# Kernel optimization log

Hardware: AMD Instinct MI355X
Metric: run time of the kernel (lower is better)

The kernel has to match this reference:

```python
import jax, jax.numpy as jnp
import numpy as np

VOCAB, DIM = 100000, 300
B, L = 4096, 200
HIDDEN, OUT = 1000, 3


def setup_inputs() -> dict:
    key = jax.random.key(0)
    k_emb, k_x, k_len, k_w1, k_b1, k_w2, k_b2 = jax.random.split(key, 7)
    emb_table = jax.random.normal(k_emb, (VOCAB, DIM), dtype=jnp.float32)
    x = jax.random.randint(k_x, (B, L), 0, VOCAB)
    lengths = jax.random.randint(k_len, (B,), 1, L + 1)  # >=1 to avoid div-by-zero
    W1 = jax.random.normal(k_w1, (2 * DIM, HIDDEN), dtype=jnp.float32) * 0.02
    b1 = jax.random.normal(k_b1, (HIDDEN,), dtype=jnp.float32) * 0.02
    W2 = jax.random.normal(k_w2, (HIDDEN, OUT), dtype=jnp.float32) * 0.02
    b2 = jax.random.normal(k_b2, (OUT,), dtype=jnp.float32) * 0.02
    return {"emb_table": emb_table, "W1": W1, "b1": b1, "W2": W2, "b2": b2,
            "x": x, "lengths": lengths}


def reference(emb_table, W1, b1, W2, b2, x, lengths):
    emb = emb_table[x]                                   # [B, L, D] gather
    # Faithful to original: mean uses sum over ALL positions (incl. padding)
    mean_pooled = jnp.sum(emb, axis=1) / lengths[:, None].astype(emb.dtype)  # [B, D]
    # Max only over the first `length` real tokens
    mask = jnp.arange(L)[None, :] < lengths[:, None]     # [B, L]
    neg_inf = jnp.array(-jnp.inf, dtype=emb.dtype)
    max_pooled = jnp.max(jnp.where(mask[:, :, None], emb, neg_inf), axis=1)  # [B, D]
    rep = jnp.concatenate([mean_pooled, max_pooled], axis=1)  # [B, 2D]
    h = jax.nn.relu(rep @ W1 + b1)                       # [B, 1000]
    return h @ W2 + b2                                   # [B, OUT]
```

## Files before the change

kernel.cpp:

```cpp
#include <hip/hip_runtime.h>
#include <math.h>

#define VOCAB  100000
#define DIM    300
#define IDIM   320
#define BB     4096
#define LL     200
#define HIDDEN 1000
#define OUTC   3
#define KT     19
#define NT     64
#define MTILES (BB / 16)

#define QSCALE (6.0f / 127.0f)
#define QINV   (127.0f / 6.0f)

#define W1_BLKS   ((KT * NT * 64 + 255) / 256)
#define INIT_BLKS ((BB * OUTC + 255) / 256)
#define CONV_BLKS ((VOCAB * 20 + 255) / 256)

typedef __attribute__((ext_vector_type(8))) short  short8;
typedef __attribute__((ext_vector_type(4))) float  floatx4;
typedef __attribute__((ext_vector_type(2))) unsigned short ushort2v;

__device__ inline ushort f2bf(float f) {
    union { float f; unsigned u; } v; v.f = f;
    unsigned u = v.u;
    u += 0x7fffu + ((u >> 16) & 1u);
    return (ushort)(u >> 16);
}
__device__ inline float4 f4max(float4 a, float4 b) {
    return make_float4(fmaxf(a.x, b.x), fmaxf(a.y, b.y), fmaxf(a.z, b.z), fmaxf(a.w, b.w));
}
__device__ inline float4 f4add(float4 a, float4 b) {
    return make_float4(a.x + b.x, a.y + b.y, a.z + b.z, a.w + b.w);
}
__device__ inline unsigned pkmax16(unsigned a, unsigned b) {
    union { unsigned u; ushort2v v; } x, y, r;
    x.u = a; y.u = b;
    r.v = __builtin_elementwise_max(x.v, y.v);
    return r.u;
}

__device__ inline int a_slot(int k, int ml) {
    const int kt = k >> 5, kk = k & 31;
    return ((kt << 6) + ml + ((kk >> 3) << 4)) * 8 + (kk & 7);
}

__device__ inline unsigned q4(float a, float b, float c, float d) {
    int q0 = min(max(__float2int_rn(a * QINV) + 128, 0), 255);
    int q1 = min(max(__float2int_rn(b * QINV) + 128, 0), 255);
    int q2 = min(max(__float2int_rn(c * QINV) + 128, 0), 255);
    int q3 = min(max(__float2int_rn(d * QINV) + 128, 0), 255);
    return (unsigned)q0 | ((unsigned)q1 << 8) | ((unsigned)q2 << 16) | ((unsigned)q3 << 24);
}

__device__ inline void acc_sm(const uint4& raw, unsigned* sLo, unsigned* sHi,
                              unsigned* mLo, unsigned* mHi) {
    const unsigned* ww = (const unsigned*)&raw;
    #pragma unroll
    for (int w = 0; w < 4; ++w) {
        const unsigned u  = ww[w];
        const unsigned lo = u & 0x00FF00FFu;
        const unsigned hi = (u >> 8) & 0x00FF00FFu;
        sLo[w] += lo;  sHi[w] += hi;
        mLo[w] = pkmax16(mLo[w], lo);
        mHi[w] = pkmax16(mHi[w], hi);
    }
}
__device__ inline void acc_s(const uint4& raw, unsigned* sLo, unsigned* sHi) {
    const unsigned* ww = (const unsigned*)&raw;
    #pragma unroll
    for (int w = 0; w < 4; ++w) {
        const unsigned u = ww[w];
        sLo[w] += u & 0x00FF00FFu;
        sHi[w] += (u >> 8) & 0x00FF00FFu;
    }
}

__global__ __launch_bounds__(256) void prep_all(
    const float* __restrict__ emb, unsigned char* __restrict__ embQ,
    const float* __restrict__ W1,  ushort* __restrict__ w1p,
    const float* __restrict__ b2,  float* __restrict__ out)
{
    const int bid = blockIdx.x;
    const int tid = threadIdx.x;
    if (bid < W1_BLKS) {
        const int g = bid * 256 + tid;
        if (g >= KT * NT * 64) return;
        const int lane = g & 63;
        const int nt   = (g >> 6) & (NT - 1);
        const int kt   = g >> 12;
        const int n    = nt * 16 + (lane & 15);
        const int kb   = kt * 32 + ((lane >> 4) << 3);
        short8 v;
        #pragma unroll
        for (int j = 0; j < 8; ++j) {
            const int k = kb + j;
            const float f = (k < 600 && n < HIDDEN) ? W1[k * HIDDEN + n] : 0.f;
            v[j] = (short)f2bf(f);
        }
        ((short8*)w1p)[g] = v;
    } else if (bid < W1_BLKS + INIT_BLKS) {
        const int g = (bid - W1_BLKS) * 256 + tid;
        if (g < BB * OUTC) out[g] = b2[g % OUTC];
    } else {
        const int g = (bid - W1_BLKS - INIT_BLKS) * 256 + tid;
        if (g >= VOCAB * 20) return;
        const int row = g / 20;
        const int c   = g - row * 20;
        const float4* rp = (const float4*)(emb + (size_t)row * DIM);
        uint4 o;
        unsigned* ow = (unsigned*)&o;
        #pragma unroll
        for (int v = 0; v < 4; ++v) {
            const int fi = 4 * c + v;
            float4 f = (fi < 75) ? rp[fi] : make_float4(0.f, 0.f, 0.f, 0.f);
            ow[v] = q4(f.x, f.y, f.z, f.w);
        }
        *(uint4*)(embQ + (size_t)g * 16) = o;
    }
}

__global__ __launch_bounds__(256, 8) void gather_pool_i8(
    const unsigned char* __restrict__ embQ,
    const int*           __restrict__ x,
    const int*           __restrict__ lengths,
    ushort*              __restrict__ repA)
{
    __shared__ int      xS[LL];
    __shared__ unsigned pS[3][20][8];
    __shared__ unsigned pM[3][20][8];

    const int tid  = threadIdx.x;
    const int lane = tid & 63;
    const int wave = tid >> 6;
    const int row  = blockIdx.x;

    for (int i = tid; i < LL; i += 256) xS[i] = x[row * LL + i];
    const int len = lengths[row];
    __syncthreads();

    const int  t0   = wave * 50;
    const int  vmax = min(max(len - t0, 0), 50);
    const bool ga   = (lane < 20);
    const bool ld   = (lane < 40);
    const int  lg   = ga ? lane : (lane - 20);
    const unsigned char* base = embQ + 16 * lg;

    unsigned sLo[4], sHi[4], mLo[4], mHi[4];
    #pragma unroll
    for (int w = 0; w < 4; ++w) { sLo[w] = sHi[w] = 0u; mLo[w] = mHi[w] = 0u; }

    const int full = vmax >> 1;
    int p = 0;
    for (; p + 2 <= full; p += 2) {
        const int tA = t0 + 2 * p;
        const int i0 = ga ? xS[tA]     : xS[tA + 1];
        const int i1 = ga ? xS[tA + 2] : xS[tA + 3];
        uint4 r0 = make_uint4(0,0,0,0), r1 = make_uint4(0,0,0,0);
        if (ld) {
            r0 = *(const uint4*)(base + (size_t)i0 * IDIM);
            r1 = *(const uint4*)(base + (size_t)i1 * IDIM);
        }
        acc_sm(r0, sLo, sHi, mLo, mHi);
        acc_sm(r1, sLo, sHi, mLo, mHi);
    }
    if (p < full) {
        const int tA = t0 + 2 * p;
        const int i0 = ga ? xS[tA] : xS[tA + 1];
        uint4 r0 = make_uint4(0,0,0,0);
        if (ld) r0 = *(const uint4*)(base + (size_t)i0 * IDIM);
        acc_sm(r0, sLo, sHi, mLo, mHi);
        ++p;
    }
    if (vmax & 1) {
        const int tA = t0 + 2 * p;
        const int i0 = ga ? xS[tA] : xS[tA + 1];
        uint4 r0 = make_uint4(0,0,0,0);
        if (ld) r0 = *(const uint4*)(base + (size_t)i0 * IDIM);
        const unsigned* ww = (const unsigned*)&r0;
        #pragma unroll
        for (int w = 0; w < 4; ++w) {
            const unsigned u  = ww[w];
            const unsigned lo = u & 0x00FF00FFu;
            const unsigned hi = (u >> 8) & 0x00FF00FFu;
            sLo[w] += lo;  sHi[w] += hi;
            if (ga) { mLo[w] = pkmax16(mLo[w], lo); mHi[w] = pkmax16(mHi[w], hi); }
        }
        ++p;
    }
    for (; p + 2 <= 25; p += 2) {
        const int tA = t0 + 2 * p;
        const int i0 = ga ? xS[tA]     : xS[tA + 1];
        const int i1 = ga ? xS[tA + 2] : xS[tA + 3];
        uint4 r0 = make_uint4(0,0,0,0), r1 = make_uint4(0,0,0,0);
        if (ld) {
            r0 = *(const uint4*)(base + (size_t)i0 * IDIM);
            r1 = *(const uint4*)(base + (size_t)i1 * IDIM);
        }
        acc_s(r0, sLo, sHi);
        acc_s(r1, sLo, sHi);
    }
    if (p < 25) {
        const int tA = t0 + 2 * p;
        const int i0 = ga ? xS[tA] : xS[tA + 1];
        uint4 r0 = make_uint4(0,0,0,0);
        if (ld) r0 = *(const uint4*)(base + (size_t)i0 * IDIM);
        acc_s(r0, sLo, sHi);
    }

    {
        const int src = ga ? (lane + 20) : lane;
        #pragma unroll
        for (int w = 0; w < 4; ++w) {
            sLo[w] += (unsigned)__shfl((int)sLo[w], src);
            sHi[w] += (unsigned)__shfl((int)sHi[w], src);
            mLo[w] = pkmax16(mLo[w], (unsigned)__shfl((int)mLo[w], src));
            mHi[w] = pkmax16(mHi[w], (unsigned)__shfl((int)mHi[w], src));
        }
    }

    if (wave != 0 && ga) {
        #pragma unroll
        for (int w = 0; w < 4; ++w) {
            pS[wave - 1][lane][w]     = sLo[w];
            pS[wave - 1][lane][4 + w] = sHi[w];
            pM[wave - 1][lane][w]     = mLo[w];
            pM[wave - 1][lane][4 + w] = mHi[w];
        }
    }
    __syncthreads();
    if (wave == 0 && ga) {
        #pragma unroll
        for (int wv = 0; wv < 3; ++wv)
            #pragma unroll
            for (int w = 0; w < 4; ++w) {
                sLo[w] += pS[wv][lane][w];
                sHi[w] += pS[wv][lane][4 + w];
                mLo[w] = pkmax16(mLo[w], pM[wv][lane][w]);
                mHi[w] = pkmax16(mHi[w], pM[wv][lane][4 + w]);
            }

        float s[16], m[16];
        #pragma unroll
        for (int w = 0; w < 4; ++w) {
            s[4*w+0] = (float)(sLo[w] & 0xFFFFu);
            s[4*w+2] = (float)(sLo[w] >> 16);
            s[4*w+1] = (float)(sHi[w] & 0xFFFFu);
            s[4*w+3] = (float)(sHi[w] >> 16);
            m[4*w+0] = (float)(mLo[w] & 0xFFFFu);
            m[4*w+2] = (float)(mLo[w] >> 16);
            m[4*w+1] = (float)(mHi[w] & 0xFFFFu);
            m[4*w+3] = (float)(mHi[w] >> 16);
        }

        const float c1 = QSCALE / (float)len;
        const int mt = row >> 4;
        const int ml = row & 15;
        ushort* rb = repA + (size_t)mt * (KT * 512);

        ushort mv[16];
        #pragma unroll
        for (int j = 0; j < 16; ++j) mv[j] = f2bf((m[j] - 128.f) * QSCALE);

        if (lane < 18) {
            #pragma unroll
            for (int h = 0; h < 2; ++h) {
                short8 q;
                #pragma unroll
                for (int j = 0; j < 8; ++j)
                    q[j] = (short)f2bf((s[8*h + j] - 25600.f) * c1);
                *(short8*)(rb + a_slot(16 * lane + 8 * h, ml)) = q;
            }
            #pragma unroll
            for (int h = 0; h < 2; ++h) {
                const int k0 = 300 + 16 * lane + 8 * h;
                *(ushort4*)(rb + a_slot(k0, ml)) =
                    make_ushort4(mv[8*h+0], mv[8*h+1], mv[8*h+2], mv[8*h+3]);
                *(ushort4*)(rb + a_slot(k0 + 4, ml)) =
                    make_ushort4(mv[8*h+4], mv[8*h+5], mv[8*h+6], mv[8*h+7]);
            }
        } else if (lane == 18) {
            short8 q;
            #pragma unroll
            for (int j = 0; j < 8; ++j) q[j] = (short)f2bf((s[j] - 25600.f) * c1);
            *(short8*)(rb + a_slot(288, ml)) = q;
            *(ushort4*)(rb + a_slot(296, ml)) =
                make_ushort4(f2bf((s[8] - 25600.f) * c1), f2bf((s[9] - 25600.f) * c1),
                             f2bf((s[10] - 25600.f) * c1), f2bf((s[11] - 25600.f) * c1));
            *(ushort4*)(rb + a_slot(588, ml)) = make_ushort4(mv[0], mv[1], mv[2], mv[3]);
            *(ushort4*)(rb + a_slot(592, ml)) = make_ushort4(mv[4], mv[5], mv[6], mv[7]);
            *(ushort4*)(rb + a_slot(596, ml)) = make_ushort4(mv[8], mv[9], mv[10], mv[11]);
            *(ushort4*)(rb + a_slot(600, ml)) = make_ushort4(0, 0, 0, 0);
        } else {
            *(ushort4*)(rb + a_slot(604, ml)) = make_ushort4(0, 0, 0, 0);
        }
    }
}

__global__ __launch_bounds__(256, 8) void gather_pool_f32(
    const float* __restrict__ emb,
    const int*   __restrict__ x,
    const int*   __restrict__ lengths,
    ushort*      __restrict__ repA)
{
    __shared__ int    xS[LL];
    __shared__ float4 pS[3][75];
    __shared__ float4 pM[3][75];

    const int tid  = threadIdx.x;
    const int lane = tid & 63;
    const int wave = tid >> 6;
    const int row  = blockIdx.x;

    for (int i = tid; i < LL; i += 256) xS[i] = x[row * LL + i];
    const int len = lengths[row];
    __syncthreads();

    const int  t0   = wave * (LL / 4);
    const int  vmax = min(max(len - t0, 0), LL / 4);
    const bool tl   = (lane < 11);
    const float4 z4 = make_float4(0.f, 0.f, 0.f, 0.f);

    float4 s4 = z4, st = z4;
    float4 m4 = make_float4(-INFINITY, -INFINITY, -INFINITY, -INFINITY);
    float4 mt = m4;

    int t = 0;
    #pragma unroll 4
    for (; t < vmax; ++t) {
        const int idx = xS[t0 + t];
        const float4* rp = (const float4*)(emb + (size_t)idx * DIM);
        float4 a = rp[lane];
        float4 b = tl ? rp[64 + lane] : z4;
        s4 = f4add(s4, a); st = f4add(st, b);
        m4 = f4max(m4, a); mt = f4max(mt, b);
    }
    #pragma unroll 4
    for (; t < LL / 4; ++t) {
        const int idx = xS[t0 + t];
        const float4* rp = (const float4*)(emb + (size_t)idx * DIM);
        float4 a = rp[lane];
        float4 b = tl ? rp[64 + lane] : z4;
        s4 = f4add(s4, a); st = f4add(st, b);
    }

    if (wave != 0) {
        pS[wave - 1][lane] = s4; pM[wave - 1][lane] = m4;
        if (tl) { pS[wave - 1][64 + lane] = st; pM[wave - 1][64 + lane] = mt; }
    }
    __syncthreads();
    if (wave == 0) {
        #pragma unroll
        for (int w = 0; w < 3; ++w) {
            s4 = f4add(s4, pS[w][lane]); m4 = f4max(m4, pM[w][lane]);
            if (tl) { st = f4add(st, pS[w][64 + lane]); mt = f4max(mt, pM[w][64 + lane]); }
        }
        const float inv = 1.0f / (float)len;
        const int mtile = row >> 4;
        const int ml    = row & 15;
        ushort* rb = repA + (size_t)mtile * (KT * 512);
        {
            ushort4 q = make_ushort4(f2bf(s4.x*inv), f2bf(s4.y*inv), f2bf(s4.z*inv), f2bf(s4.w*inv));
            *(ushort4*)(rb + a_slot(4 * lane, ml)) = q;
        }
        {
            ushort4 q = make_ushort4(f2bf(m4.x), f2bf(m4.y), f2bf(m4.z), f2bf(m4.w));
            *(ushort4*)(rb + a_slot(300 + 4 * lane, ml)) = q;
        }
        if (tl) {
            ushort4 q1 = make_ushort4(f2bf(st.x*inv), f2bf(st.y*inv), f2bf(st.z*inv), f2bf(st.w*inv));
            *(ushort4*)(rb + a_slot(256 + 4 * lane, ml)) = q1;
            ushort4 q2 = make_ushort4(f2bf(mt.x), f2bf(mt.y), f2bf(mt.z), f2bf(mt.w));
            *(ushort4*)(rb + a_slot(556 + 4 * lane, ml)) = q2;
        }
        if (lane >= 56) rb[a_slot(600 + (lane - 56), ml)] = 0;
    }
}

__global__ __launch_bounds__(256, 4) void mlp_mfma(
    const ushort* __restrict__ w1p,
    const ushort* __restrict__ repA,
    const float*  __restrict__ bias1,
    const float*  __restrict__ W2,
    float*        __restrict__ out)
{
    __shared__ short8 aS[2 * KT * 64];

    const int tid  = threadIdx.x;
    const int lane = tid & 63;
    const int wave = tid >> 6;
    const int mp   = blockIdx.x >> 3;
    const int e    = blockIdx.x & 7;

    {
        const short8* ap = (const short8*)(repA + (size_t)(2 * mp) * (KT * 512));
        for (int i = tid; i < 2 * KT * 64; i += 256) aS[i] = ap[i];
    }
    __syncthreads();

    const int nt0 = e * 8 + wave;
    const int nt1 = nt0 + 4;
    const short8* bp = (const short8*)w1p;

    floatx4 acc[2][2];
    #pragma unroll
    for (int mi = 0; mi < 2; ++mi)
        #pragma unroll
        for (int s = 0; s < 2; ++s) acc[mi][s] = (floatx4){0.f, 0.f, 0.f, 0.f};

    #pragma unroll
    for (int kt = 0; kt < KT; ++kt) {
        const short8 av0 = aS[kt * 64 + lane];
        const short8 av1 = aS[KT * 64 + kt * 64 + lane];
        const short8 bv0 = bp[(kt * NT + nt0) * 64 + lane];
        const short8 bv1 = bp[(kt * NT + nt1) * 64 + lane];
        acc[0][0] = __builtin_amdgcn_mfma_f32_16x16x32_bf16(av0, bv0, acc[0][0], 0, 0, 0);
        acc[0][1] = __builtin_amdgcn_mfma_f32_16x16x32_bf16(av0, bv1, acc[0][1], 0, 0, 0);
        acc[1][0] = __builtin_amdgcn_mfma_f32_16x16x32_bf16(av1, bv0, acc[1][0], 0, 0, 0);
        acc[1][1] = __builtin_amdgcn_mfma_f32_16x16x32_bf16(av1, bv1, acc[1][1], 0, 0, 0);
    }
    __syncthreads();
    float* red = (float*)aS;

    float po[2][4][3];
    #pragma unroll
    for (int mi = 0; mi < 2; ++mi)
        #pragma unroll
        for (int rg = 0; rg < 4; ++rg)
            #pragma unroll
            for (int j = 0; j < OUTC; ++j) po[mi][rg][j] = 0.f;

    #pragma unroll
    for (int s = 0; s < 2; ++s) {
        const int n = (s ? nt1 : nt0) * 16 + (lane & 15);
        const bool valid = (n < HIDDEN);
        const float bb  = bias1[valid ? n : 0];
        const float w20 = valid ? W2[n * 3 + 0] : 0.f;
        const float w21 = valid ? W2[n * 3 + 1] : 0.f;
        const float w22 = valid ? W2[n * 3 + 2] : 0.f;
        #pragma unroll
        for (int mi = 0; mi < 2; ++mi)
            #pragma unroll
            for (int rg = 0; rg < 4; ++rg) {
                const float h = fmaxf(acc[mi][s][rg] + bb, 0.f);
                po[mi][rg][0] = fmaf(h, w20, po[mi][rg][0]);
                po[mi][rg][1] = fmaf(h, w21, po[mi][rg][1]);
                po[mi][rg][2] = fmaf(h, w22, po[mi][rg][2]);
            }
    }

    #pragma unroll
    for (int mi = 0; mi < 2; ++mi)
        #pragma unroll
        for (int rg = 0; rg < 4; ++rg)
            #pragma unroll
            for (int j = 0; j < OUTC; ++j) {
                float v = po[mi][rg][j];
                v += __shfl_xor(v, 1);
                v += __shfl_xor(v, 2);
                v += __shfl_xor(v, 4);
                v += __shfl_xor(v, 8);
                if ((lane & 15) == 0)
                    red[(wave * 32 + mi * 16 + (lane >> 4) * 4 + rg) * 3 + j] = v;
            }
    __syncthreads();

    if (tid < 32 * OUTC) {
        const int m = tid / OUTC, j = tid % OUTC;
        const float s = red[(0 * 32 + m) * 3 + j] + red[(1 * 32 + m) * 3 + j]
                      + red[(2 * 32 + m) * 3 + j] + red[(3 * 32 + m) * 3 + j];
        atomicAdd(&out[(size_t)(mp * 32 + m) * OUTC + j], s);
    }
}

extern "C" void kernel_launch(void* const* d_in, const int* in_sizes, int n_in,
                              void* d_out, int out_size, void* d_ws, size_t ws_size,
                              hipStream_t stream) {
    const float* emb = (const float*)d_in[0];
    const float* W1  = (const float*)d_in[1];
    const float* b1  = (const float*)d_in[2];
    const float* W2  = (const float*)d_in[3];
    const float* b2  = (const float*)d_in[4];
    const int*   x   = (const int*)d_in[5];
    const int*   len = (const int*)d_in[6];
    float* out = (float*)d_out;

    const size_t W1P_ELTS  = (size_t)KT * NT * 64 * 8;
    const size_t REPA_ELTS = (size_t)MTILES * KT * 512;
    ushort* w1p  = (ushort*)d_ws;
    ushort* repA = w1p + W1P_ELTS;
    unsigned char* embQ = (unsigned char*)(repA + REPA_ELTS);
    const size_t need = (W1P_ELTS + REPA_ELTS) * 2 + (size_t)VOCAB * IDIM;
    const bool doConv = (ws_size >= need);

    const int prepGrid = W1_BLKS + INIT_BLKS + (doConv ? CONV_BLKS : 0);
    hipLaunchKernelGGL(prep_all, dim3(prepGrid), dim3(256), 0, stream,
                       emb, embQ, W1, w1p, b2, out);
    if (doConv) {
        hipLaunchKernelGGL(gather_pool_i8, dim3(BB), dim3(256), 0, stream,
                           embQ, x, len, repA);
    } else {
        hipLaunchKernelGGL(gather_pool_f32, dim3(BB), dim3(256), 0, stream,
                           emb, x, len, repA);
    }
    hipLaunchKernelGGL(mlp_mfma, dim3((MTILES / 2) * 8), dim3(256), 0, stream,
                       w1p, repA, b1, W2, out);
}
```

Baseline: 256.9 us.

## Fuse MLP into gather kernel via last-block-per-tile election

The int8 gather/pool kernel now counts finished rows per 16-row tile with an atomic counter. The last block to finish a tile then runs the full MLP for that tile with MFMA and atomically adds the results to the output, which removes the separate MLP launch and its pass over repA. The fallback MLP kernel is retiled to 16-row tiles split four ways across hidden columns. The cost is that only 256 elected blocks do the MLP, each computing all 1000 hidden units serially with 4 waves. Lowering the launch bound to 4 blocks per SM may also reduce gather occupancy.

```diff
diff --git a/kernel.cpp b/kernel.cpp
--- a/kernel.cpp
+++ b/kernel.cpp
@@ -81,7 +81,8 @@
 __global__ __launch_bounds__(256) void prep_all(
     const float* __restrict__ emb, unsigned char* __restrict__ embQ,
     const float* __restrict__ W1,  ushort* __restrict__ w1p,
-    const float* __restrict__ b2,  float* __restrict__ out)
+    const float* __restrict__ b2,  float* __restrict__ out,
+    int* __restrict__ cnt)
 {
     const int bid = blockIdx.x;
     const int tid = threadIdx.x;
@@ -104,6 +105,7 @@
     } else if (bid < W1_BLKS + INIT_BLKS) {
         const int g = (bid - W1_BLKS) * 256 + tid;
         if (g < BB * OUTC) out[g] = b2[g % OUTC];
+        if (g < MTILES) cnt[g] = 0;
     } else {
         const int g = (bid - W1_BLKS - INIT_BLKS) * 256 + tid;
         if (g >= VOCAB * 20) return;
@@ -122,15 +124,23 @@
     }
 }
 
-__global__ __launch_bounds__(256, 8) void gather_pool_i8(
+__global__ __launch_bounds__(256, 4) void gather_mlp_i8(
     const unsigned char* __restrict__ embQ,
     const int*           __restrict__ x,
     const int*           __restrict__ lengths,
-    ushort*              __restrict__ repA)
+    ushort*              __restrict__ repA,
+    const ushort*        __restrict__ w1p,
+    const float*         __restrict__ bias1,
+    const float*         __restrict__ W2,
+    float*               __restrict__ out,
+    int*                 __restrict__ cnt)
 {
-    __shared__ int      xS[LL];
-    __shared__ unsigned pS[3][20][8];
-    __shared__ unsigned pM[3][20][8];
+    __shared__ __attribute__((aligned(16))) char shbuf[KT * 64 * 16];
+    __shared__ int electFlag;
+
+    int*      xS  = (int*)shbuf;
+    unsigned* pSf = (unsigned*)(shbuf + 800);
+    unsigned* pMf = (unsigned*)(shbuf + 2720);
 
     const int tid  = threadIdx.x;
     const int lane = tid & 63;
@@ -224,10 +234,10 @@
     if (wave != 0 && ga) {
         #pragma unroll
         for (int w = 0; w < 4; ++w) {
-            pS[wave - 1][lane][w]     = sLo[w];
-            pS[wave - 1][lane][4 + w] = sHi[w];
-            pM[wave - 1][lane][w]     = mLo[w];
-            pM[wave - 1][lane][4 + w] = mHi[w];
+            pSf[((wave - 1) * 20 + lane) * 8 + w]     = sLo[w];
+            pSf[((wave - 1) * 20 + lane) * 8 + 4 + w] = sHi[w];
+            pMf[((wave - 1) * 20 + lane) * 8 + w]     = mLo[w];
+            pMf[((wave - 1) * 20 + lane) * 8 + 4 + w] = mHi[w];
         }
     }
     __syncthreads();
@@ -236,10 +246,10 @@
         for (int wv = 0; wv < 3; ++wv)
             #pragma unroll
             for (int w = 0; w < 4; ++w) {
-                sLo[w] += pS[wv][lane][w];
-                sHi[w] += pS[wv][lane][4 + w];
-                mLo[w] = pkmax16(mLo[w], pM[wv][lane][w]);
-                mHi[w] = pkmax16(mHi[w], pM[wv][lane][4 + w]);
+                sLo[w] += pSf[(wv * 20 + lane) * 8 + w];
+                sHi[w] += pSf[(wv * 20 + lane) * 8 + 4 + w];
+                mLo[w] = pkmax16(mLo[w], pMf[(wv * 20 + lane) * 8 + w]);
+                mHi[w] = pkmax16(mHi[w], pMf[(wv * 20 + lane) * 8 + 4 + w]);
             }
 
         float s[16], m[16];
@@ -297,6 +307,88 @@
             *(ushort4*)(rb + a_slot(604, ml)) = make_ushort4(0, 0, 0, 0);
         }
     }
+
+    if (tid == 0) {
+        __threadfence();
+        electFlag = (atomicAdd(&cnt[row >> 4], 1) == 15) ? 1 : 0;
+    }
+    __syncthreads();
+    if (!electFlag) return;
+    __threadfence();
+
+    const int g = row >> 4;
+    short8* aS = (short8*)shbuf;
+    {
+        const short8* ap = (const short8*)(repA + (size_t)g * (KT * 512));
+        for (int i = tid; i < KT * 64; i += 256) aS[i] = ap[i];
+    }
+    __syncthreads();
+
+    float po[4][3];
+    #pragma unroll
+    for (int rg = 0; rg < 4; ++rg)
+        #pragma unroll
+        for (int j = 0; j < OUTC; ++j) po[rg][j] = 0.f;
+
+    const short8* bp = (const short8*)w1p;
+    #pragma unroll
+    for (int c = 0; c < 4; ++c) {
+        const int nt0 = wave * 16 + c * 4;
+        floatx4 acc[4];
+        #pragma unroll
+        for (int s2 = 0; s2 < 4; ++s2) acc[s2] = (floatx4){0.f, 0.f, 0.f, 0.f};
+        #pragma unroll
+        for (int kt = 0; kt < KT; ++kt) {
+            const short8 av  = aS[kt * 64 + lane];
+            const short8 b0  = bp[(kt * NT + nt0 + 0) * 64 + lane];
+            const short8 b1v = bp[(kt * NT + nt0 + 1) * 64 + lane];
+            const short8 b2v = bp[(kt * NT + nt0 + 2) * 64 + lane];
+            const short8 b3v = bp[(kt * NT + nt0 + 3) * 64 + lane];
+            acc[0] = __builtin_amdgcn_mfma_f32_16x16x32_bf16(av, b0,  acc[0], 0, 0, 0);
+            acc[1] = __builtin_amdgcn_mfma_f32_16x16x32_bf16(av, b1v, acc[1], 0, 0, 0);
+            acc[2] = __builtin_amdgcn_mfma_f32_16x16x32_bf16(av, b2v, acc[2], 0, 0, 0);
+            acc[3] = __builtin_amdgcn_mfma_f32_16x16x32_bf16(av, b3v, acc[3], 0, 0, 0);
+        }
+        #pragma unroll
+        for (int s2 = 0; s2 < 4; ++s2) {
+            const int n = (nt0 + s2) * 16 + (lane & 15);
+            const bool valid = (n < HIDDEN);
+            const float bb  = bias1[valid ? n : 0];
+            const float w20 = valid ? W2[n * 3 + 0] : 0.f;
+            const float w21 = valid ? W2[n * 3 + 1] : 0.f;
+            const float w22 = valid ? W2[n * 3 + 2] : 0.f;
+            #pragma unroll
+            for (int rg = 0; rg < 4; ++rg) {
+                const float h = fmaxf(acc[s2][rg] + bb, 0.f);
+                po[rg][0] = fmaf(h, w20, po[rg][0]);
+                po[rg][1] = fmaf(h, w21, po[rg][1]);
+                po[rg][2] = fmaf(h, w22, po[rg][2]);
+            }
+        }
+    }
+
+    __syncthreads();
+    float* red = (float*)shbuf;
+    #pragma unroll
+    for (int rg = 0; rg < 4; ++rg)
+        #pragma unroll
+        for (int j = 0; j < OUTC; ++j) {
+            float v = po[rg][j];
+            v += __shfl_xor(v, 1);
+            v += __shfl_xor(v, 2);
+            v += __shfl_xor(v, 4);
+            v += __shfl_xor(v, 8);
+            if ((lane & 15) == 0)
+                red[(wave * 16 + (lane >> 4) * 4 + rg) * 3 + j] = v;
+        }
+    __syncthreads();
+
+    if (tid < 16 * OUTC) {
+        const int m = tid / OUTC, j = tid % OUTC;
+        const float sv = red[(0 * 16 + m) * 3 + j] + red[(1 * 16 + m) * 3 + j]
+                       + red[(2 * 16 + m) * 3 + j] + red[(3 * 16 + m) * 3 + j];
+        atomicAdd(&out[(size_t)(g * 16 + m) * OUTC + j], sv);
+    }
 }
 
 __global__ __launch_bounds__(256, 8) void gather_pool_f32(
@@ -386,92 +478,82 @@
     const float*  __restrict__ W2,
     float*        __restrict__ out)
 {
-    __shared__ short8 aS[2 * KT * 64];
+    __shared__ short8 aS[KT * 64];
+    __shared__ float  red[4][16][3];
 
     const int tid  = threadIdx.x;
     const int lane = tid & 63;
     const int wave = tid >> 6;
-    const int mp   = blockIdx.x >> 3;
-    const int e    = blockIdx.x & 7;
+    const int mt   = blockIdx.x >> 2;
+    const int q    = blockIdx.x & 3;
 
     {
-        const short8* ap = (const short8*)(repA + (size_t)(2 * mp) * (KT * 512));
-        for (int i = tid; i < 2 * KT * 64; i += 256) aS[i] = ap[i];
-    }
-    __syncthreads();
-
-    const int nt0 = e * 8 + wave;
-    const int nt1 = nt0 + 4;
+        const short8* ap = (const short8*)(repA + (size_t)mt * (KT * 512));
+        for (int i = tid; i < KT * 64; i += 256) aS[i] = ap[i];
+    }
+    __syncthreads();
+
+    const int nt0 = q * 16 + wave * 4;
     const short8* bp = (const short8*)w1p;
 
-    floatx4 acc[2][2];
-    #pragma unroll
-    for (int mi = 0; mi < 2; ++mi)
-        #pragma unroll
-        for (int s = 0; s < 2; ++s) acc[mi][s] = (floatx4){0.f, 0.f, 0.f, 0.f};
+    floatx4 acc[4];
+    #pragma unroll
+    for (int s = 0; s < 4; ++s) acc[s] = (floatx4){0.f, 0.f, 0.f, 0.f};
 
     #pragma unroll
     for (int kt = 0; kt < KT; ++kt) {
-        const short8 av0 = aS[kt * 64 + lane];
-        const short8 av1 = aS[KT * 64 + kt * 64 + lane];
-        const short8 bv0 = bp[(kt * NT + nt0) * 64 + lane];
-        const short8 bv1 = bp[(kt * NT + nt1) * 64 + lane];
-        acc[0][0] = __builtin_amdgcn_mfma_f32_16x16x32_bf16(av0, bv0, acc[0][0], 0, 0, 0);
-        acc[0][1] = __builtin_amdgcn_mfma_f32_16x16x32_bf16(av0, bv1, acc[0][1], 0, 0, 0);
-        acc[1][0] = __builtin_amdgcn_mfma_f32_16x16x32_bf16(av1, bv0, acc[1][0], 0, 0, 0);
-        acc[1][1] = __builtin_amdgcn_mfma_f32_16x16x32_bf16(av1, bv1, acc[1][1], 0, 0, 0);
-    }
-    __syncthreads();
-    float* red = (float*)aS;
-
-    float po[2][4][3];
-    #pragma unroll
-    for (int mi = 0; mi < 2; ++mi)
-        #pragma unroll
-        for (int rg = 0; rg < 4; ++rg)
-            #pragma unroll
-            for (int j = 0; j < OUTC; ++j) po[mi][rg][j] = 0.f;
-
-    #pragma unroll
-    for (int s = 0; s < 2; ++s) {
-        const int n = (s ? nt1 : nt0) * 16 + (lane & 15);
+        const short8 av = aS[kt * 64 + lane];
+        const short8 b0 = bp[(kt * NT + nt0 + 0) * 64 + lane];
+        const short8 b1v = bp[(kt * NT + nt0 + 1) * 64 + lane];
+        const short8 b2v = bp[(kt * NT + nt0 + 2) * 64 + lane];
+        const short8 b3 = bp[(kt * NT + nt0 + 3) * 64 + lane];
+        acc[0] = __builtin_amdgcn_mfma_f32_16x16x32_bf16(av, b0,  acc[0], 0, 0, 0);
+        acc[1] = __builtin_amdgcn_mfma_f32_16x16x32_bf16(av, b1v, acc[1], 0, 0, 0);
+        acc[2] = __builtin_amdgcn_mfma_f32_16x16x32_bf16(av, b2v, acc[2], 0, 0, 0);
+        acc[3] = __builtin_amdgcn_mfma_f32_16x16x32_bf16(av, b3,  acc[3], 0, 0, 0);
+    }
+
+    float po[4][3];
+    #pragma unroll
+    for (int rg = 0; rg < 4; ++rg)
+        #pragma unroll
+        for (int j = 0; j < OUTC; ++j) po[rg][j] = 0.f;
+
+    #pragma unroll
+    for (int s = 0; s < 4; ++s) {
+        const int n = (nt0 + s) * 16 + (lane & 15);
         const bool valid = (n < HIDDEN);
         const float bb  = bias1[valid ? n : 0];
         const float w20 = valid ? W2[n * 3 + 0] : 0.f;
         const float w21 = valid ? W2[n * 3 + 1] : 0.f;
         const float w22 = valid ? W2[n * 3 + 2] : 0.f;
         #pragma unroll
-        for (int mi = 0; mi < 2; ++mi)
-            #pragma unroll
-            for (int rg = 0; rg < 4; ++rg) {
-                const float h = fmaxf(acc[mi][s][rg] + bb, 0.f);
-                po[mi][rg][0] = fmaf(h, w20, po[mi][rg][0]);
-                po[mi][rg][1] = fmaf(h, w21, po[mi][rg][1]);
-                po[mi][rg][2] = fmaf(h, w22, po[mi][rg][2]);
-            }
-    }
-
-    #pragma unroll
-    for (int mi = 0; mi < 2; ++mi)
-        #pragma unroll
-        for (int rg = 0; rg < 4; ++rg)
-            #pragma unroll
-            for (int j = 0; j < OUTC; ++j) {
-                float v = po[mi][rg][j];
-                v += __shfl_xor(v, 1);
-                v += __shfl_xor(v, 2);
-                v += __shfl_xor(v, 4);
-                v += __shfl_xor(v, 8);
-                if ((lane & 15) == 0)
-                    red[(wave * 32 + mi * 16 + (lane >> 4) * 4 + rg) * 3 + j] = v;
-            }
-    __syncthreads();
-
-    if (tid < 32 * OUTC) {
+        for (int rg = 0; rg < 4; ++rg) {
+            const float h = fmaxf(acc[s][rg] + bb, 0.f);
+            po[rg][0] = fmaf(h, w20, po[rg][0]);
+            po[rg][1] = fmaf(h, w21, po[rg][1]);
+            po[rg][2] = fmaf(h, w22, po[rg][2]);
+        }
+    }
+
+    #pragma unroll
+    for (int rg = 0; rg < 4; ++rg) {
+        #pragma unroll
+        for (int j = 0; j < OUTC; ++j) {
+            float v = po[rg][j];
+            v += __shfl_xor(v, 1);
+            v += __shfl_xor(v, 2);
+            v += __shfl_xor(v, 4);
+            v += __shfl_xor(v, 8);
+            if ((lane & 15) == 0) red[wave][(lane >> 4) * 4 + rg][j] = v;
+        }
+    }
+    __syncthreads();
+
+    if (tid < 16 * OUTC) {
         const int m = tid / OUTC, j = tid % OUTC;
-        const float s = red[(0 * 32 + m) * 3 + j] + red[(1 * 32 + m) * 3 + j]
-                      + red[(2 * 32 + m) * 3 + j] + red[(3 * 32 + m) * 3 + j];
-        atomicAdd(&out[(size_t)(mp * 32 + m) * OUTC + j], s);
+        const float s = red[0][m][j] + red[1][m][j] + red[2][m][j] + red[3][m][j];
+        atomicAdd(&out[(size_t)(mt * 16 + m) * OUTC + j], s);
     }
 }
 
@@ -492,19 +574,21 @@
     ushort* w1p  = (ushort*)d_ws;
     ushort* repA = w1p + W1P_ELTS;
     unsigned char* embQ = (unsigned char*)(repA + REPA_ELTS);
-    const size_t need = (W1P_ELTS + REPA_ELTS) * 2 + (size_t)VOCAB * IDIM;
+    int* cnt = (int*)(embQ + (size_t)VOCAB * IDIM);
+    const size_t need = (W1P_ELTS + REPA_ELTS) * 2 + (size_t)VOCAB * IDIM
+                      + MTILES * sizeof(int);
     const bool doConv = (ws_size >= need);
 
     const int prepGrid = W1_BLKS + INIT_BLKS + (doConv ? CONV_BLKS : 0);
     hipLaunchKernelGGL(prep_all, dim3(prepGrid), dim3(256), 0, stream,
-                       emb, embQ, W1, w1p, b2, out);
+                       emb, embQ, W1, w1p, b2, out, cnt);
     if (doConv) {
-        hipLaunchKernelGGL(gather_pool_i8, dim3(BB), dim3(256), 0, stream,
-                           embQ, x, len, repA);
+        hipLaunchKernelGGL(gather_mlp_i8, dim3(BB), dim3(256), 0, stream,
+                           embQ, x, len, repA, w1p, b1, W2, out, cnt);
     } else {
         hipLaunchKernelGGL(gather_pool_f32, dim3(BB), dim3(256), 0, stream,
                            emb, x, len, repA);
-    }
-    hipLaunchKernelGGL(mlp_mfma, dim3((MTILES / 2) * 8), dim3(256), 0, stream,
-                       w1p, repA, b1, W2, out);
-}
+        hipLaunchKernelGGL(mlp_mfma, dim3(MTILES * 4), dim3(256), 0, stream,
+                           w1p, repA, b1, W2, out);
+    }
+}
```

Result: slower. 737.6 us (+187.1%).
